# Optimization experiments

Hardware: AMD Instinct MI355X
Metric: run time of the kernel (lower is better)

## Reference

```python
import jax, jax.numpy as jnp
import numpy as np

G = 32            # gridsize
N = G * G         # num_nodes = 1024
F_IN = 32         # input_dim
H = 256           # hidden_dim
L = 4             # n_layers
B = 64            # batch
MID = F_IN + L * H
MIN_VAL = -10000000.0
EPS_LN = 1e-5
EPS_BN = 1e-5


def _grid_edges():
    ids = np.arange(N).reshape(G, G)
    hs, hd = ids[:, :-1].ravel(), ids[:, 1:].ravel()
    vs, vd = ids[:-1, :].ravel(), ids[1:, :].ravel()
    src = np.concatenate([hs, hd, vs, vd]).astype(np.int32)
    dst = np.concatenate([hd, hs, vd, vs]).astype(np.int32)
    return jnp.asarray(src), jnp.asarray(dst)


def setup_inputs() -> dict:
    key = jax.random.key(0)
    ks = jax.random.split(key, 16)
    mask_f = jax.random.bernoulli(ks[0], 0.7, (B, N)).astype(jnp.float32)
    feats = jax.random.normal(ks[1], (B, N * F_IN), dtype=jnp.float32)
    observations = jnp.concatenate([mask_f, feats], axis=1)
    src, dst = _grid_edges()
    def lin(k, fi, fo):
        return jax.random.normal(k, (fi, fo), dtype=jnp.float32) / np.sqrt(fi)
    W0 = lin(ks[2], F_IN, H); b0 = jnp.zeros((H,), jnp.float32)
    g0 = jnp.ones((H,), jnp.float32); be0 = jnp.zeros((H,), jnp.float32)
    Ws = jax.random.normal(ks[3], (L - 1, H, H), jnp.float32) / np.sqrt(H)
    bs = jnp.zeros((L - 1, H), jnp.float32)
    gs = jnp.ones((L - 1, H), jnp.float32); bes = jnp.zeros((L - 1, H), jnp.float32)
    W1 = lin(ks[4], MID, 2 * H); b1 = jnp.zeros((2 * H,), jnp.float32)
    bn_g = jnp.ones((2 * H,), jnp.float32); bn_b = jnp.zeros((2 * H,), jnp.float32)
    bn_m = jax.random.normal(ks[5], (2 * H,), jnp.float32) * 0.1
    bn_v = jax.random.uniform(ks[6], (2 * H,), jnp.float32, 0.5, 1.5)
    W2 = lin(ks[7], 2 * H, 1); b2 = jnp.zeros((1,), jnp.float32)
    return {"observations": observations, "src": src, "dst": dst,
            "W0": W0, "b0": b0, "g0": g0, "be0": be0,
            "Ws": Ws, "bs": bs, "gs": gs, "bes": bes,
            "W1": W1, "b1": b1, "bn_g": bn_g, "bn_b": bn_b,
            "bn_m": bn_m, "bn_v": bn_v, "W2": W2, "b2": b2}


def _layer_norm(z, g, b):
    mu = z.mean(-1, keepdims=True)
    var = z.var(-1, keepdims=True)
    return (z - mu) / jnp.sqrt(var + EPS_LN) * g + b


def reference(observations, src, dst, W0, b0, g0, be0, Ws, bs, gs, bes,
              W1, b1, bn_g, bn_b, bn_m, bn_v, W2, b2):
    mask = observations[:, :N] != 0.0                      # [B,N] bool action mask
    x = observations[:, N:].reshape(B, N, F_IN)            # node features
    outs = [x]
    h = x
    for l in range(L):
        # GIN with eps=-1: (1+eps)*x_i vanishes -> mlp(sum of neighbor features)
        agg = jnp.zeros_like(h).at[:, dst, :].add(h[:, src, :])
        W, bb, g, be = ((W0, b0, g0, be0) if l == 0
                        else (Ws[l - 1], bs[l - 1], gs[l - 1], bes[l - 1]))
        h = jax.nn.relu(_layer_norm(agg @ W + bb, g, be))  # mlp ReLU; outer .relu() is idempotent
        outs.append(h)
    xc = jnp.concatenate(outs, axis=-1).reshape(B * N, MID)
    z = xc @ W1 + b1
    z = (z - bn_m) / jnp.sqrt(bn_v + EPS_BN) * bn_g + bn_b  # BatchNorm1d eval mode
    z = jax.nn.relu(z)                                       # dropout off in eval
    y = (z @ W2 + b2).reshape(B, N)
    return jnp.where(mask, y, MIN_VAL)
```

## Files before the change

kernel.cpp:

```cpp
#include <hip/hip_runtime.h>
#include <stdint.h>

#define FIN 32
#define HD 256
#define MIDK 1056
#define HF 512
#define MROWS 65536
#define OBS_STRIDE 33792

typedef float f32x2 __attribute__((ext_vector_type(2)));
typedef float f32x4 __attribute__((ext_vector_type(4)));

__device__ __forceinline__ unsigned char f2fp8(float f) {
    return (unsigned char)(__builtin_amdgcn_cvt_pk_fp8_f32(f, f, 0, false) & 0xff);
}
__device__ __forceinline__ unsigned pack4fp8(float a, float b, float c, float d) {
    int w = __builtin_amdgcn_cvt_pk_fp8_f32(a, b, 0, false);
    return (unsigned)__builtin_amdgcn_cvt_pk_fp8_f32(c, d, w, true);
}

__device__ __forceinline__ void glds16(const void* g, void* l) {
    __builtin_amdgcn_global_load_lds(
        (const __attribute__((address_space(1))) unsigned int*)g,
        (__attribute__((address_space(3))) unsigned int*)l,
        16, 0, 0);
}

__global__ void k_prep(const float* __restrict__ obs, unsigned char* __restrict__ xb,
                       const float* __restrict__ b1, const float* __restrict__ g,
                       const float* __restrict__ bb, const float* __restrict__ m,
                       const float* __restrict__ v,
                       float* __restrict__ cs, float* __restrict__ cb) {
    int t = blockIdx.x * 256 + threadIdx.x;
    {
        int base = t * 8;
        int b = base >> 15;
        int off = base & 32767;
        const float* p = obs + (size_t)b * OBS_STRIDE + 1024 + off;
        float4 f0 = *(const float4*)p;
        float4 f1 = *(const float4*)(p + 4);
        uint2 o;
        o.x = pack4fp8(f0.x, f0.y, f0.z, f0.w);
        o.y = pack4fp8(f1.x, f1.y, f1.z, f1.w);
        *(uint2*)(xb + base) = o;
    }
    if (t < HF) {
        float s = g[t] * rsqrtf(v[t] + 1e-5f);
        cs[t] = s;
        cb[t] = (b1[t] - m[t]) * s + bb[t];
    }
}

__device__ __forceinline__ void trans_tile(const float* __restrict__ src,
                                           unsigned char* __restrict__ dst,
                                           int NN, int k0, int n0, int t, int mode) {
    __shared__ float tl[32][33];
    int ir = t >> 5, ic = t & 31;
#pragma unroll
    for (int p = 0; p < 4; ++p)
        tl[p * 8 + ir][ic] = src[(size_t)(k0 + p * 8 + ir) * NN + n0 + ic];
    __syncthreads();
#pragma unroll
    for (int p = 0; p < 4; ++p) {
        int n = n0 + p * 8 + ir;
        int k = k0 + ic;
        size_t off;
        if (mode == 0)
            off = (size_t)(((k >> 5) << 9) + (((k >> 4) & 1) << 8) + n) * 16 + (k & 15);
        else
            off = (size_t)(((k >> 6) << 11) + (((k >> 4) & 3) << 9) + n) * 16 + (k & 15);
        dst[off] = f2fp8(tl[ic][p * 8 + ir]);
    }
}

__global__ __launch_bounds__(256) void k_prep_w(
        const float* __restrict__ W0, const float* __restrict__ Ws,
        const float* __restrict__ W1,
        unsigned char* __restrict__ Wt0, unsigned char* __restrict__ WtL,
        unsigned char* __restrict__ WtF) {
    int b = blockIdx.x, t = threadIdx.x;
    if (b < 528) {
        int kt = b >> 4, nt = b & 15;
        trans_tile(W1, WtF, HF, kt * 32, nt * 32, t, 1);
    } else if (b < 720) {
        int j = b - 528;
        int l = j >> 6, r = j & 63;
        trans_tile(Ws + l * 65536, WtL + l * 65536, HD, (r >> 3) * 32, (r & 7) * 32, t, 0);
    } else {
        int nt = b - 720;
        trans_tile(W0, Wt0, HD, 0, nt * 32, t, 0);
    }
}

template <int K>
__global__ __launch_bounds__(256) void k_layer(
        const unsigned char* __restrict__ Hin,
        const unsigned char* __restrict__ Wt,
        const float* __restrict__ bias, const float* __restrict__ gamma,
        const float* __restrict__ beta, unsigned char* __restrict__ Hout) {
    constexpr int KB = K / 32;
    __shared__ __align__(16) unsigned char Agg[(K / 16) * 64 * 16];
    __shared__ __align__(16) unsigned char Bs[2][512 * 16];
    __shared__ float ls[64], lss[64];
    const int t = threadIdx.x;
    const int w = t >> 6, lane = t & 63, quad = lane >> 4, l15 = lane & 15;
    const int m0 = ((blockIdx.x & 7) * 128 + (blockIdx.x >> 3)) * 64;
    if (t < 64) { ls[t] = 0.f; lss[t] = 0.f; }

    {
        const int r = t & 63, c4 = t >> 6;
        const int gm = m0 + r;
        const int node = gm & 1023;
        const int rr = node >> 5, cc = node & 31;
        const size_t rowBase = (size_t)(gm & ~1023);
        for (int kb = c4; kb < KB; kb += 4) {
            float s[32];
#pragma unroll
            for (int i = 0; i < 32; ++i) s[i] = 0.f;
            auto addn = [&](int nn) {
                const uint4* p = (const uint4*)(Hin + (rowBase + nn) * (size_t)K + kb * 32);
                uint4 u0 = p[0], u1 = p[1];
                unsigned uu[8] = {u0.x, u0.y, u0.z, u0.w, u1.x, u1.y, u1.z, u1.w};
#pragma unroll
                for (int i = 0; i < 8; ++i) {
                    f32x2 lo = __builtin_amdgcn_cvt_pk_f32_fp8(uu[i], false);
                    f32x2 hi = __builtin_amdgcn_cvt_pk_f32_fp8(uu[i], true);
                    s[4 * i + 0] += lo.x; s[4 * i + 1] += lo.y;
                    s[4 * i + 2] += hi.x; s[4 * i + 3] += hi.y;
                }
            };
            if (cc > 0)  addn(node - 1);
            if (cc < 31) addn(node + 1);
            if (rr > 0)  addn(node - 32);
            if (rr < 31) addn(node + 32);
            unsigned ow[8];
#pragma unroll
            for (int i = 0; i < 8; ++i)
                ow[i] = pack4fp8(s[4 * i], s[4 * i + 1], s[4 * i + 2], s[4 * i + 3]);
            ((uint4*)Agg)[(2 * kb) * 64 + r]     = make_uint4(ow[0], ow[1], ow[2], ow[3]);
            ((uint4*)Agg)[(2 * kb + 1) * 64 + r] = make_uint4(ow[4], ow[5], ow[6], ow[7]);
        }
    }
#pragma unroll
    for (int i = 0; i < 2; ++i) {
        int s = t + i * 256;
        glds16(Wt + (size_t)s * 16, Bs[0] + (s & ~63) * 16);
    }
    __syncthreads();

    f32x4 acc[4][4] = {};
#pragma unroll
    for (int kb = 0; kb < KB; ++kb) {
        if (kb + 1 < KB) {
#pragma unroll
            for (int i = 0; i < 2; ++i) {
                int s = t + i * 256;
                glds16(Wt + ((size_t)(kb + 1) * 512 + s) * 16, Bs[(kb + 1) & 1] + (s & ~63) * 16);
            }
        }
        const unsigned char* bb = Bs[kb & 1];
        long long af[4], bf[4];
#pragma unroll
        for (int mt = 0; mt < 4; ++mt)
            af[mt] = *(const long long*)(Agg + (((kb * 2 + (quad >> 1)) * 64 + mt * 16 + l15) * 16) + (quad & 1) * 8);
#pragma unroll
        for (int nt = 0; nt < 4; ++nt)
            bf[nt] = *(const long long*)(bb + (((quad >> 1) * 256 + w * 64 + nt * 16 + l15) * 16) + (quad & 1) * 8);
#pragma unroll
        for (int mt = 0; mt < 4; ++mt)
#pragma unroll
            for (int nt = 0; nt < 4; ++nt)
                acc[mt][nt] = __builtin_amdgcn_mfma_f32_16x16x32_fp8_fp8(af[mt], bf[nt], acc[mt][nt], 0, 0, 0);
        __syncthreads();
    }

#pragma unroll
    for (int mt = 0; mt < 4; ++mt) {
        float s0 = 0, s1 = 0, s2 = 0, s3 = 0, q0 = 0, q1 = 0, q2 = 0, q3 = 0;
#pragma unroll
        for (int nt = 0; nt < 4; ++nt) {
            int col = w * 64 + nt * 16 + l15;
            float bv = bias[col];
            f32x4 v = acc[mt][nt];
            v.x += bv; v.y += bv; v.z += bv; v.w += bv;
            acc[mt][nt] = v;
            s0 += v.x; q0 += v.x * v.x;
            s1 += v.y; q1 += v.y * v.y;
            s2 += v.z; q2 += v.z * v.z;
            s3 += v.w; q3 += v.w * v.w;
        }
#pragma unroll
        for (int msk = 1; msk < 16; msk <<= 1) {
            s0 += __shfl_xor(s0, msk); q0 += __shfl_xor(q0, msk);
            s1 += __shfl_xor(s1, msk); q1 += __shfl_xor(q1, msk);
            s2 += __shfl_xor(s2, msk); q2 += __shfl_xor(q2, msk);
            s3 += __shfl_xor(s3, msk); q3 += __shfl_xor(q3, msk);
        }
        if (l15 == 0) {
            int rl = mt * 16 + quad * 4;
            atomicAdd(&ls[rl + 0], s0); atomicAdd(&lss[rl + 0], q0);
            atomicAdd(&ls[rl + 1], s1); atomicAdd(&lss[rl + 1], q1);
            atomicAdd(&ls[rl + 2], s2); atomicAdd(&lss[rl + 2], q2);
            atomicAdd(&ls[rl + 3], s3); atomicAdd(&lss[rl + 3], q3);
        }
    }
    __syncthreads();
#pragma unroll
    for (int mt = 0; mt < 4; ++mt) {
        int rl = mt * 16 + quad * 4;
        float mu0 = ls[rl + 0] * (1.f / 256.f), mu1 = ls[rl + 1] * (1.f / 256.f);
        float mu2 = ls[rl + 2] * (1.f / 256.f), mu3 = ls[rl + 3] * (1.f / 256.f);
        float rs0 = rsqrtf(lss[rl + 0] * (1.f / 256.f) - mu0 * mu0 + 1e-5f);
        float rs1 = rsqrtf(lss[rl + 1] * (1.f / 256.f) - mu1 * mu1 + 1e-5f);
        float rs2 = rsqrtf(lss[rl + 2] * (1.f / 256.f) - mu2 * mu2 + 1e-5f);
        float rs3 = rsqrtf(lss[rl + 3] * (1.f / 256.f) - mu3 * mu3 + 1e-5f);
#pragma unroll
        for (int nt = 0; nt < 4; ++nt) {
            int col = w * 64 + nt * 16 + l15;
            float g = gamma[col], be = beta[col];
            f32x4 v = acc[mt][nt];
            size_t rb = (size_t)(m0 + mt * 16 + quad * 4) * HD + col;
            Hout[rb]          = f2fp8(fmaxf((v.x - mu0) * rs0 * g + be, 0.f));
            Hout[rb + HD]     = f2fp8(fmaxf((v.y - mu1) * rs1 * g + be, 0.f));
            Hout[rb + 2 * HD] = f2fp8(fmaxf((v.z - mu2) * rs2 * g + be, 0.f));
            Hout[rb + 3 * HD] = f2fp8(fmaxf((v.w - mu3) * rs3 * g + be, 0.f));
        }
    }
}

__global__ __launch_bounds__(512) void k_final(
        const unsigned char* __restrict__ xb,
        const unsigned char* __restrict__ h0, const unsigned char* __restrict__ h1,
        const unsigned char* __restrict__ h2, const unsigned char* __restrict__ h3,
        const unsigned char* __restrict__ WtF,
        const float* __restrict__ cs, const float* __restrict__ cb,
        const float* __restrict__ W2, const float* __restrict__ b2,
        const float* __restrict__ obs, float* __restrict__ out) {
    __shared__ __align__(16) unsigned char As[256 * 16];
    __shared__ __align__(16) unsigned char Bsm[2048 * 16];
    __shared__ float yred[64];
    const int t = threadIdx.x;
    const int w = t >> 6, lane = t & 63, quad = lane >> 4, l15 = lane & 15;
    const int wr = w >> 2, wc = w & 3;
    const int m0 = ((blockIdx.x & 7) * 128 + (blockIdx.x >> 3)) * 64;
    if (t < 64) yred[t] = 0.f;

    const unsigned char* hbuf[4] = {h0, h1, h2, h3};
    f32x4 acc[2][8] = {};

    for (int iter = 0; iter < 17; ++iter) {
        const int kb = iter * 64;
        const int steps = (iter < 16) ? 2 : 1;
        if (t < steps * 128) {
            int h = t >> 6, r = t & 63;
            int k = kb + h * 16;
            const unsigned char* src;
            if (k < 32) src = xb + (size_t)(m0 + r) * FIN + k;
            else { int j = k - 32; src = hbuf[j >> 8] + (size_t)(m0 + r) * HD + (j & 255); }
            glds16(src, As + (t & ~63) * 16);
        }
        for (int i = 0; i < steps * 2; ++i) {
            int s = t + i * 512;
            glds16(WtF + ((size_t)iter * 2048 + s) * 16, Bsm + (s & ~63) * 16);
        }
        __syncthreads();
#pragma unroll 2
        for (int s2 = 0; s2 < steps; ++s2) {
            long long af[2], bf[8];
#pragma unroll
            for (int mt = 0; mt < 2; ++mt)
                af[mt] = *(const long long*)(As + (((s2 * 2 + (quad >> 1)) * 64 + wr * 32 + mt * 16 + l15) * 16) + (quad & 1) * 8);
#pragma unroll
            for (int nt = 0; nt < 8; ++nt)
                bf[nt] = *(const long long*)(Bsm + (((s2 * 2 + (quad >> 1)) * 512 + wc * 128 + nt * 16 + l15) * 16) + (quad & 1) * 8);
#pragma unroll
            for (int mt = 0; mt < 2; ++mt)
#pragma unroll
                for (int nt = 0; nt < 8; ++nt)
                    acc[mt][nt] = __builtin_amdgcn_mfma_f32_16x16x32_fp8_fp8(af[mt], bf[nt], acc[mt][nt], 0, 0, 0);
        }
        __syncthreads();
    }

#pragma unroll
    for (int mt = 0; mt < 2; ++mt) {
        float p0 = 0, p1 = 0, p2 = 0, p3 = 0;
#pragma unroll
        for (int nt = 0; nt < 8; ++nt) {
            int col = wc * 128 + nt * 16 + l15;
            float sc = cs[col], sb = cb[col], w2 = W2[col];
            f32x4 v = acc[mt][nt];
            p0 += fmaxf(v.x * sc + sb, 0.f) * w2;
            p1 += fmaxf(v.y * sc + sb, 0.f) * w2;
            p2 += fmaxf(v.z * sc + sb, 0.f) * w2;
            p3 += fmaxf(v.w * sc + sb, 0.f) * w2;
        }
#pragma unroll
        for (int msk = 1; msk < 16; msk <<= 1) {
            p0 += __shfl_xor(p0, msk);
            p1 += __shfl_xor(p1, msk);
            p2 += __shfl_xor(p2, msk);
            p3 += __shfl_xor(p3, msk);
        }
        if (l15 == 0) {
            int rl = wr * 32 + mt * 16 + quad * 4;
            atomicAdd(&yred[rl + 0], p0);
            atomicAdd(&yred[rl + 1], p1);
            atomicAdd(&yred[rl + 2], p2);
            atomicAdd(&yred[rl + 3], p3);
        }
    }
    __syncthreads();
    if (t < 64) {
        int gm = m0 + t;
        float mk = obs[(size_t)(gm >> 10) * OBS_STRIDE + (gm & 1023)];
        out[gm] = (mk != 0.f) ? yred[t] + b2[0] : -10000000.0f;
    }
}

extern "C" void kernel_launch(void* const* d_in, const int* in_sizes, int n_in,
                              void* d_out, int out_size, void* d_ws, size_t ws_size,
                              hipStream_t stream) {
    const float* obs = (const float*)d_in[0];
    const float* W0  = (const float*)d_in[3];
    const float* b0  = (const float*)d_in[4];
    const float* g0  = (const float*)d_in[5];
    const float* be0 = (const float*)d_in[6];
    const float* Ws  = (const float*)d_in[7];
    const float* bs  = (const float*)d_in[8];
    const float* gs  = (const float*)d_in[9];
    const float* bes = (const float*)d_in[10];
    const float* W1  = (const float*)d_in[11];
    const float* b1  = (const float*)d_in[12];
    const float* bng = (const float*)d_in[13];
    const float* bnb = (const float*)d_in[14];
    const float* bnm = (const float*)d_in[15];
    const float* bnv = (const float*)d_in[16];
    const float* W2  = (const float*)d_in[17];
    const float* b2  = (const float*)d_in[18];
    float* out = (float*)d_out;

    char* ws = (char*)d_ws;
    unsigned char* xb  = (unsigned char*)(ws);
    unsigned char* h0  = (unsigned char*)(ws +  2097152);
    unsigned char* h1  = (unsigned char*)(ws + 18874368);
    unsigned char* h2  = (unsigned char*)(ws + 35651584);
    unsigned char* h3  = (unsigned char*)(ws + 52428800);
    unsigned char* Wt0 = (unsigned char*)(ws + 69206016);
    unsigned char* WtL = (unsigned char*)(ws + 69214208);
    unsigned char* WtF = (unsigned char*)(ws + 69410816);
    float* cs = (float*)(ws + 69951488);
    float* cb = (float*)(ws + 69953536);

    k_prep<<<1024, 256, 0, stream>>>(obs, xb, b1, bng, bnb, bnm, bnv, cs, cb);
    k_prep_w<<<728, 256, 0, stream>>>(W0, Ws, W1, Wt0, WtL, WtF);

    k_layer<FIN><<<1024, 256, 0, stream>>>(xb, Wt0, b0, g0, be0, h0);
    k_layer<HD> <<<1024, 256, 0, stream>>>(h0, WtL,              bs,       gs,       bes,       h1);
    k_layer<HD> <<<1024, 256, 0, stream>>>(h1, WtL + 65536,      bs + 256, gs + 256, bes + 256, h2);
    k_layer<HD> <<<1024, 256, 0, stream>>>(h2, WtL + 2 * 65536,  bs + 512, gs + 512, bes + 512, h3);

    k_final<<<1024, 512, 0, stream>>>(xb, h0, h1, h2, h3, WtF, cs, cb, W2, b2, obs, out);
}
```

Baseline: 263.2 us.

## Fuse GIN layers into a persistent kernel with grid barriers and pad LDS

Merges the input fp8 conversion and the four GIN layer launches into one kernel of 1024 blocks. The blocks synchronise through an atomic-counter grid barrier in workspace, which k_prep_w resets. BatchNorm constant folding also moves into k_prep_w. LDS tiles for A and B get padded row strides (66/258/514 instead of 64/256/512) to reduce bank conflicts. This removes several kernel launch gaps, but it depends on all 1024 blocks being co-resident (launch_bounds 256,4 on 256 CUs); otherwise the spin barrier could deadlock. Spinning also adds cost per barrier.

```diff
diff --git a/kernel.cpp b/kernel.cpp
--- a/kernel.cpp
+++ b/kernel.cpp
@@ -7,6 +7,7 @@
 #define HF 512
 #define MROWS 65536
 #define OBS_STRIDE 33792
+#define NBLK 1024
 
 typedef float f32x2 __attribute__((ext_vector_type(2)));
 typedef float f32x4 __attribute__((ext_vector_type(4)));
@@ -26,29 +27,17 @@
         16, 0, 0);
 }
 
-__global__ void k_prep(const float* __restrict__ obs, unsigned char* __restrict__ xb,
-                       const float* __restrict__ b1, const float* __restrict__ g,
-                       const float* __restrict__ bb, const float* __restrict__ m,
-                       const float* __restrict__ v,
-                       float* __restrict__ cs, float* __restrict__ cb) {
-    int t = blockIdx.x * 256 + threadIdx.x;
-    {
-        int base = t * 8;
-        int b = base >> 15;
-        int off = base & 32767;
-        const float* p = obs + (size_t)b * OBS_STRIDE + 1024 + off;
-        float4 f0 = *(const float4*)p;
-        float4 f1 = *(const float4*)(p + 4);
-        uint2 o;
-        o.x = pack4fp8(f0.x, f0.y, f0.z, f0.w);
-        o.y = pack4fp8(f1.x, f1.y, f1.z, f1.w);
-        *(uint2*)(xb + base) = o;
-    }
-    if (t < HF) {
-        float s = g[t] * rsqrtf(v[t] + 1e-5f);
-        cs[t] = s;
-        cb[t] = (b1[t] - m[t]) * s + bb[t];
-    }
+__device__ __forceinline__ void gbar(int* bar, int idx) {
+    __syncthreads();
+    if (threadIdx.x == 0) {
+        __threadfence();
+        atomicAdd(&bar[idx], 1);
+        while (__hip_atomic_load(&bar[idx], __ATOMIC_RELAXED,
+                                 __HIP_MEMORY_SCOPE_AGENT) < NBLK)
+            __builtin_amdgcn_s_sleep(8);
+        __threadfence();
+    }
+    __syncthreads();
 }
 
 __device__ __forceinline__ void trans_tile(const float* __restrict__ src,
@@ -77,7 +66,11 @@
         const float* __restrict__ W0, const float* __restrict__ Ws,
         const float* __restrict__ W1,
         unsigned char* __restrict__ Wt0, unsigned char* __restrict__ WtL,
-        unsigned char* __restrict__ WtF) {
+        unsigned char* __restrict__ WtF,
+        const float* __restrict__ b1, const float* __restrict__ g,
+        const float* __restrict__ bb, const float* __restrict__ m,
+        const float* __restrict__ v,
+        float* __restrict__ cs, float* __restrict__ cb, int* __restrict__ bar) {
     int b = blockIdx.x, t = threadIdx.x;
     if (b < 528) {
         int kt = b >> 4, nt = b & 15;
@@ -86,25 +79,31 @@
         int j = b - 528;
         int l = j >> 6, r = j & 63;
         trans_tile(Ws + l * 65536, WtL + l * 65536, HD, (r >> 3) * 32, (r & 7) * 32, t, 0);
-    } else {
+    } else if (b < 728) {
         int nt = b - 720;
         trans_tile(W0, Wt0, HD, 0, nt * 32, t, 0);
+    } else {
+        int i = (b - 728) * 256 + t;
+        if (i < HF) {
+            float s = g[i] * rsqrtf(v[i] + 1e-5f);
+            cs[i] = s;
+            cb[i] = (b1[i] - m[i]) * s + bb[i];
+        }
+        if (b == 728 && t < 16) bar[t] = 0;
     }
 }
 
 template <int K>
-__global__ __launch_bounds__(256) void k_layer(
-        const unsigned char* __restrict__ Hin,
+__device__ __forceinline__ void layer_body(
+        int m0, int t, const unsigned char* __restrict__ Hin,
         const unsigned char* __restrict__ Wt,
         const float* __restrict__ bias, const float* __restrict__ gamma,
-        const float* __restrict__ beta, unsigned char* __restrict__ Hout) {
+        const float* __restrict__ beta, unsigned char* __restrict__ Hout,
+        unsigned char* Agg, unsigned char* Bs0, unsigned char* Bs1,
+        float* ls, float* lss) {
     constexpr int KB = K / 32;
-    __shared__ __align__(16) unsigned char Agg[(K / 16) * 64 * 16];
-    __shared__ __align__(16) unsigned char Bs[2][512 * 16];
-    __shared__ float ls[64], lss[64];
-    const int t = threadIdx.x;
     const int w = t >> 6, lane = t & 63, quad = lane >> 4, l15 = lane & 15;
-    const int m0 = ((blockIdx.x & 7) * 128 + (blockIdx.x >> 3)) * 64;
+    const int q1 = quad >> 1, q0 = quad & 1;
     if (t < 64) { ls[t] = 0.f; lss[t] = 0.f; }
 
     {
@@ -137,35 +136,33 @@
 #pragma unroll
             for (int i = 0; i < 8; ++i)
                 ow[i] = pack4fp8(s[4 * i], s[4 * i + 1], s[4 * i + 2], s[4 * i + 3]);
-            ((uint4*)Agg)[(2 * kb) * 64 + r]     = make_uint4(ow[0], ow[1], ow[2], ow[3]);
-            ((uint4*)Agg)[(2 * kb + 1) * 64 + r] = make_uint4(ow[4], ow[5], ow[6], ow[7]);
-        }
-    }
-#pragma unroll
-    for (int i = 0; i < 2; ++i) {
-        int s = t + i * 256;
-        glds16(Wt + (size_t)s * 16, Bs[0] + (s & ~63) * 16);
-    }
+            ((uint4*)Agg)[(2 * kb) * 66 + r]     = make_uint4(ow[0], ow[1], ow[2], ow[3]);
+            ((uint4*)Agg)[(2 * kb + 1) * 66 + r] = make_uint4(ow[4], ow[5], ow[6], ow[7]);
+        }
+    }
+#pragma unroll
+    for (int i = 0; i < 2; ++i)
+        glds16(Wt + ((size_t)i * 256 + t) * 16, Bs0 + ((size_t)i * 258 + (t & ~63)) * 16);
     __syncthreads();
 
     f32x4 acc[4][4] = {};
 #pragma unroll
     for (int kb = 0; kb < KB; ++kb) {
+        unsigned char* nb = (kb & 1) ? Bs0 : Bs1;
         if (kb + 1 < KB) {
 #pragma unroll
-            for (int i = 0; i < 2; ++i) {
-                int s = t + i * 256;
-                glds16(Wt + ((size_t)(kb + 1) * 512 + s) * 16, Bs[(kb + 1) & 1] + (s & ~63) * 16);
-            }
-        }
-        const unsigned char* bb = Bs[kb & 1];
+            for (int i = 0; i < 2; ++i)
+                glds16(Wt + (((size_t)(kb + 1) * 512) + i * 256 + t) * 16,
+                       nb + ((size_t)i * 258 + (t & ~63)) * 16);
+        }
+        const unsigned char* bb = (kb & 1) ? Bs1 : Bs0;
         long long af[4], bf[4];
 #pragma unroll
         for (int mt = 0; mt < 4; ++mt)
-            af[mt] = *(const long long*)(Agg + (((kb * 2 + (quad >> 1)) * 64 + mt * 16 + l15) * 16) + (quad & 1) * 8);
+            af[mt] = *(const long long*)(Agg + ((2 * kb + q1) * 66 + mt * 16 + l15) * 16 + q0 * 8);
 #pragma unroll
         for (int nt = 0; nt < 4; ++nt)
-            bf[nt] = *(const long long*)(bb + (((quad >> 1) * 256 + w * 64 + nt * 16 + l15) * 16) + (quad & 1) * 8);
+            bf[nt] = *(const long long*)(bb + ((size_t)(q1 * 258 + w * 64 + nt * 16 + l15)) * 16 + q0 * 8);
 #pragma unroll
         for (int mt = 0; mt < 4; ++mt)
 #pragma unroll
@@ -176,7 +173,7 @@
 
 #pragma unroll
     for (int mt = 0; mt < 4; ++mt) {
-        float s0 = 0, s1 = 0, s2 = 0, s3 = 0, q0 = 0, q1 = 0, q2 = 0, q3 = 0;
+        float s0 = 0, s1 = 0, s2 = 0, s3 = 0, u0 = 0, u1 = 0, u2 = 0, u3 = 0;
 #pragma unroll
         for (int nt = 0; nt < 4; ++nt) {
             int col = w * 64 + nt * 16 + l15;
@@ -184,24 +181,24 @@
             f32x4 v = acc[mt][nt];
             v.x += bv; v.y += bv; v.z += bv; v.w += bv;
             acc[mt][nt] = v;
-            s0 += v.x; q0 += v.x * v.x;
-            s1 += v.y; q1 += v.y * v.y;
-            s2 += v.z; q2 += v.z * v.z;
-            s3 += v.w; q3 += v.w * v.w;
+            s0 += v.x; u0 += v.x * v.x;
+            s1 += v.y; u1 += v.y * v.y;
+            s2 += v.z; u2 += v.z * v.z;
+            s3 += v.w; u3 += v.w * v.w;
         }
 #pragma unroll
         for (int msk = 1; msk < 16; msk <<= 1) {
-            s0 += __shfl_xor(s0, msk); q0 += __shfl_xor(q0, msk);
-            s1 += __shfl_xor(s1, msk); q1 += __shfl_xor(q1, msk);
-            s2 += __shfl_xor(s2, msk); q2 += __shfl_xor(q2, msk);
-            s3 += __shfl_xor(s3, msk); q3 += __shfl_xor(q3, msk);
+            s0 += __shfl_xor(s0, msk); u0 += __shfl_xor(u0, msk);
+            s1 += __shfl_xor(s1, msk); u1 += __shfl_xor(u1, msk);
+            s2 += __shfl_xor(s2, msk); u2 += __shfl_xor(u2, msk);
+            s3 += __shfl_xor(s3, msk); u3 += __shfl_xor(u3, msk);
         }
         if (l15 == 0) {
             int rl = mt * 16 + quad * 4;
-            atomicAdd(&ls[rl + 0], s0); atomicAdd(&lss[rl + 0], q0);
-            atomicAdd(&ls[rl + 1], s1); atomicAdd(&lss[rl + 1], q1);
-            atomicAdd(&ls[rl + 2], s2); atomicAdd(&lss[rl + 2], q2);
-            atomicAdd(&ls[rl + 3], s3); atomicAdd(&lss[rl + 3], q3);
+            atomicAdd(&ls[rl + 0], s0); atomicAdd(&lss[rl + 0], u0);
+            atomicAdd(&ls[rl + 1], s1); atomicAdd(&lss[rl + 1], u1);
+            atomicAdd(&ls[rl + 2], s2); atomicAdd(&lss[rl + 2], u2);
+            atomicAdd(&ls[rl + 3], s3); atomicAdd(&lss[rl + 3], u3);
         }
     }
     __syncthreads();
@@ -228,6 +225,41 @@
     }
 }
 
+__global__ __launch_bounds__(256, 4) void k_net(
+        const float* __restrict__ obs, unsigned char* __restrict__ xb,
+        const unsigned char* __restrict__ Wt0, const unsigned char* __restrict__ WtL,
+        const float* __restrict__ b0, const float* __restrict__ g0, const float* __restrict__ be0,
+        const float* __restrict__ bs, const float* __restrict__ gs, const float* __restrict__ bes,
+        unsigned char* __restrict__ h0, unsigned char* __restrict__ h1,
+        unsigned char* __restrict__ h2, unsigned char* __restrict__ h3,
+        int* __restrict__ bar) {
+    __shared__ __align__(16) unsigned char Agg[1056 * 16];
+    __shared__ __align__(16) unsigned char Bs0[516 * 16];
+    __shared__ __align__(16) unsigned char Bs1[516 * 16];
+    __shared__ float ls[64], lss[64];
+    const int bid = blockIdx.x, t = threadIdx.x;
+    const int m0 = ((bid & 7) * 128 + (bid >> 3)) * 64;
+
+    {
+        int b = m0 >> 10, node0 = m0 & 1023;
+        const float* p = obs + (size_t)b * OBS_STRIDE + 1024 + node0 * FIN + t * 8;
+        float4 f0 = *(const float4*)p;
+        float4 f1 = *(const float4*)(p + 4);
+        uint2 o;
+        o.x = pack4fp8(f0.x, f0.y, f0.z, f0.w);
+        o.y = pack4fp8(f1.x, f1.y, f1.z, f1.w);
+        *(uint2*)(xb + (size_t)m0 * FIN + t * 8) = o;
+    }
+    gbar(bar, 0);
+    layer_body<FIN>(m0, t, xb, Wt0, b0, g0, be0, h0, Agg, Bs0, Bs1, ls, lss);
+    gbar(bar, 1);
+    layer_body<HD>(m0, t, h0, WtL, bs, gs, bes, h1, Agg, Bs0, Bs1, ls, lss);
+    gbar(bar, 2);
+    layer_body<HD>(m0, t, h1, WtL + 65536, bs + 256, gs + 256, bes + 256, h2, Agg, Bs0, Bs1, ls, lss);
+    gbar(bar, 3);
+    layer_body<HD>(m0, t, h2, WtL + 131072, bs + 512, gs + 512, bes + 512, h3, Agg, Bs0, Bs1, ls, lss);
+}
+
 __global__ __launch_bounds__(512) void k_final(
         const unsigned char* __restrict__ xb,
         const unsigned char* __restrict__ h0, const unsigned char* __restrict__ h1,
@@ -236,11 +268,12 @@
         const float* __restrict__ cs, const float* __restrict__ cb,
         const float* __restrict__ W2, const float* __restrict__ b2,
         const float* __restrict__ obs, float* __restrict__ out) {
-    __shared__ __align__(16) unsigned char As[256 * 16];
-    __shared__ __align__(16) unsigned char Bsm[2048 * 16];
+    __shared__ __align__(16) unsigned char As[264 * 16];
+    __shared__ __align__(16) unsigned char Bsm[2056 * 16];
     __shared__ float yred[64];
     const int t = threadIdx.x;
     const int w = t >> 6, lane = t & 63, quad = lane >> 4, l15 = lane & 15;
+    const int q1 = quad >> 1, q0 = quad & 1;
     const int wr = w >> 2, wc = w & 3;
     const int m0 = ((blockIdx.x & 7) * 128 + (blockIdx.x >> 3)) * 64;
     if (t < 64) yred[t] = 0.f;
@@ -255,24 +288,23 @@
             int h = t >> 6, r = t & 63;
             int k = kb + h * 16;
             const unsigned char* src;
-            if (k < 32) src = xb + (size_t)(m0 + r) * FIN + k;
-            else { int j = k - 32; src = hbuf[j >> 8] + (size_t)(m0 + r) * HD + (j & 255); }
-            glds16(src, As + (t & ~63) * 16);
-        }
-        for (int i = 0; i < steps * 2; ++i) {
-            int s = t + i * 512;
-            glds16(WtF + ((size_t)iter * 2048 + s) * 16, Bsm + (s & ~63) * 16);
-        }
+            if (k < FIN) src = xb + (size_t)(m0 + r) * FIN + k;
+            else { int j = k - FIN; src = hbuf[j >> 8] + (size_t)(m0 + r) * HD + (j & 255); }
+            glds16(src, As + (size_t)(t >> 6) * 66 * 16);
+        }
+        for (int i = 0; i < steps * 2; ++i)
+            glds16(WtF + ((size_t)iter * 2048 + i * 512 + t) * 16,
+                   Bsm + ((size_t)i * 514 + (t & ~63)) * 16);
         __syncthreads();
 #pragma unroll 2
         for (int s2 = 0; s2 < steps; ++s2) {
             long long af[2], bf[8];
 #pragma unroll
             for (int mt = 0; mt < 2; ++mt)
-                af[mt] = *(const long long*)(As + (((s2 * 2 + (quad >> 1)) * 64 + wr * 32 + mt * 16 + l15) * 16) + (quad & 1) * 8);
+                af[mt] = *(const long long*)(As + ((s2 * 2 + q1) * 66 + wr * 32 + mt * 16 + l15) * 16 + q0 * 8);
 #pragma unroll
             for (int nt = 0; nt < 8; ++nt)
-                bf[nt] = *(const long long*)(Bsm + (((s2 * 2 + (quad >> 1)) * 512 + wc * 128 + nt * 16 + l15) * 16) + (quad & 1) * 8);
+                bf[nt] = *(const long long*)(Bsm + ((size_t)((s2 * 2 + q1) * 514 + wc * 128 + nt * 16 + l15)) * 16 + q0 * 8);
 #pragma unroll
             for (int mt = 0; mt < 2; ++mt)
 #pragma unroll
@@ -351,14 +383,12 @@
     unsigned char* WtF = (unsigned char*)(ws + 69410816);
     float* cs = (float*)(ws + 69951488);
     float* cb = (float*)(ws + 69953536);
-
-    k_prep<<<1024, 256, 0, stream>>>(obs, xb, b1, bng, bnb, bnm, bnv, cs, cb);
-    k_prep_w<<<728, 256, 0, stream>>>(W0, Ws, W1, Wt0, WtL, WtF);
-
-    k_layer<FIN><<<1024, 256, 0, stream>>>(xb, Wt0, b0, g0, be0, h0);
-    k_layer<HD> <<<1024, 256, 0, stream>>>(h0, WtL,              bs,       gs,       bes,       h1);
-    k_layer<HD> <<<1024, 256, 0, stream>>>(h1, WtL + 65536,      bs + 256, gs + 256, bes + 256, h2);
-    k_layer<HD> <<<1024, 256, 0, stream>>>(h2, WtL + 2 * 65536,  bs + 512, gs + 512, bes + 512, h3);
-
+    int*  bar = (int*)  (ws + 69955584);
+
+    k_prep_w<<<730, 256, 0, stream>>>(W0, Ws, W1, Wt0, WtL, WtF,
+                                      b1, bng, bnb, bnm, bnv, cs, cb, bar);
+    k_net<<<NBLK, 256, 0, stream>>>(obs, xb, Wt0, WtL,
+                                    b0, g0, be0, bs, gs, bes,
+                                    h0, h1, h2, h3, bar);
     k_final<<<1024, 512, 0, stream>>>(xb, h0, h1, h2, h3, WtF, cs, cb, W2, b2, obs, out);
 }
```

Measured after the change: 830.8 us. 216% more time.
